# Kernel optimization log

Hardware: AMD Instinct MI355X
Metric: run time of the kernel (lower is better)

The kernel has to match this reference:

```python
import jax, jax.numpy as jnp
import numpy as np

B, T, D, H = 2, 2048, 1024, 16
DH = D // H


def setup_inputs() -> dict:
    key = jax.random.key(0)
    ks = jax.random.split(key, 8)
    s = 1.0 / np.sqrt(D)  # xavier-ish scale
    return {
        "query": jax.random.normal(ks[0], (B, T, D), jnp.float32),
        "key": jax.random.normal(ks[1], (B, T, D), jnp.float32),
        "value": jax.random.normal(ks[2], (B, T, D), jnp.float32),
        "Wq": jax.random.normal(ks[3], (D, D), jnp.float32) * s,
        "bq": jnp.zeros((D,), jnp.float32),
        "Wk": jax.random.normal(ks[4], (D, D), jnp.float32) * s,
        "bk": jnp.zeros((D,), jnp.float32),
        "Wv": jax.random.normal(ks[5], (D, D), jnp.float32) * s,
        "bv": jnp.zeros((D,), jnp.float32),
        "Wo": jax.random.normal(ks[6], (D, D), jnp.float32) * s,
        "bo": jnp.zeros((D,), jnp.float32),
        # causal mask (B, T, T); True = attend
        "mask": jnp.broadcast_to(jnp.tril(jnp.ones((T, T), bool)), (B, T, T)),
    }


def _split_heads(x):  # (B, T, D) -> (B, H, T, Dh)
    return x.reshape(B, T, H, DH).transpose(0, 2, 1, 3)


def reference(query, key, value, Wq, bq, Wk, bk, Wv, bv, Wo, bo, mask):
    q = _split_heads(query @ Wq + bq)
    k = _split_heads(key @ Wk + bk)
    v = _split_heads(value @ Wv + bv)
    scores = jnp.einsum("bhqd,bhkd->bhqk", q, k) / jnp.sqrt(jnp.float32(DH))
    scores = jnp.where(mask[:, None, :, :], scores, -jnp.inf)
    w = jax.nn.softmax(scores, axis=-1)
    out = jnp.einsum("bhqk,bhkd->bhqd", w, v)
    out = out.transpose(0, 2, 1, 3).reshape(B, T, D)  # merge heads
    return out @ Wo + bo
```

## Files before the change

kernel.cpp:

```cpp
#include <hip/hip_runtime.h>

typedef unsigned short u16;
typedef __attribute__((ext_vector_type(4))) float f32x4;
typedef __attribute__((ext_vector_type(8))) short bf16x8;

#define MFMA16(a,b,c) __builtin_amdgcn_mfma_f32_16x16x32_bf16((a),(b),(c),0,0,0)

__device__ inline u16 f2bf(float f){
  union { float f; unsigned u; } v; v.f = f;
  unsigned r = v.u + 0x7FFFu + ((v.u >> 16) & 1u);
  return (u16)(r >> 16);
}
__device__ inline u16 f2bf_fast(float f){
  union { float f; unsigned u; } v; v.f = f;
  return (u16)((v.u + 0x8000u) >> 16);
}

typedef const __attribute__((address_space(1))) unsigned int* gas_ptr;
typedef __attribute__((address_space(3))) unsigned int* las_ptr;
__device__ inline void gload_lds16(const u16* g, u16* l){
  __builtin_amdgcn_global_load_lds((gas_ptr)(const void*)g, (las_ptr)(void*)l, 16, 0, 0);
}

struct CvtArgs { const float* x[3]; u16* y[3]; };
__global__ void k_cvt3(CvtArgs a, int n4){
  const float* x = a.x[blockIdx.y];
  u16* y = a.y[blockIdx.y];
  int i = blockIdx.x*blockDim.x + threadIdx.x;
  if (i < n4){
    float4 v = ((const float4*)x)[i];
    ushort4 o;
    o.x = f2bf(v.x); o.y = f2bf(v.y); o.z = f2bf(v.z); o.w = f2bf(v.w);
    ((ushort4*)y)[i] = o;
  }
}

struct TwbArgs { const float* W[4]; u16* Wt[4]; };
__global__ void k_twb4(TwbArgs a){
  __shared__ u16 t[32][33];
  const float* W = a.W[blockIdx.z];
  u16* Wt = a.Wt[blockIdx.z];
  int kb = blockIdx.x*32, nb = blockIdx.y*32;
  int tx = threadIdx.x, ty = threadIdx.y;
  #pragma unroll
  for (int i=0;i<32;i+=8)
    t[ty+i][tx] = f2bf(W[(size_t)(kb+ty+i)*1024 + nb+tx]);
  __syncthreads();
  #pragma unroll
  for (int i=0;i<32;i+=8)
    Wt[(size_t)(nb+ty+i)*1024 + kb+tx] = t[tx][ty+i];
}

__global__ void k_tv(const u16* __restrict__ V, u16* __restrict__ VT){
  __shared__ u16 t[32][33];
  int tb = blockIdx.x*32;
  int db = blockIdx.y*32;
  int bh = blockIdx.z;
  int b = bh>>4, h = bh&15;
  int tx = threadIdx.x, ty = threadIdx.y;
  #pragma unroll
  for (int i=0;i<32;i+=8)
    t[ty+i][tx] = V[(size_t)(b*2048 + tb+ty+i)*1024 + h*64 + db+tx];
  __syncthreads();
  #pragma unroll
  for (int i=0;i<32;i+=8)
    VT[(size_t)(bh*64 + db+ty+i)*2048 + tb+tx] = t[tx][ty+i];
}

struct GemmArgs3 { const u16* A[3]; const u16* Bt[3]; const float* bias[3]; u16* C[3]; };
__global__ __launch_bounds__(256) void k_gemm3(GemmArgs3 g){
  const int N=1024, K=1024;
  int flat = blockIdx.x + (blockIdx.y<<5) + (blockIdx.z<<8);
  int swz = (flat&7)*96 + (flat>>3);
  int by = swz & 7, bx = (swz>>3) & 31, bz = swz >> 8;
  const u16* A = g.A[bz]; const u16* Bt = g.Bt[bz];
  const float* bias = g.bias[bz]; u16* C = g.C[bz];
  __shared__ __attribute__((aligned(16))) u16 As[128*64];
  __shared__ __attribute__((aligned(16))) u16 Bs[128*64];
  const int tid  = threadIdx.x;
  const int wave = tid>>6, lane = tid&63;
  const int lo = lane&15, hi = lane>>4;
  const int row0 = bx*128, col0 = by*128;
  const int wm = (wave>>1)*64, wn = (wave&1)*64;
  f32x4 acc[4][4];
  #pragma unroll
  for (int i=0;i<4;i++)
    #pragma unroll
    for (int j=0;j<4;j++) acc[i][j] = (f32x4){0.f,0.f,0.f,0.f};

  for (int k0=0; k0<K; k0+=64){
    #pragma unroll
    for (int r=0;r<4;r++){
      int c = r*256 + tid;
      gload_lds16(A  + (size_t)(row0 + (c>>3))*K + k0 + (c&7)*8, As + c*8);
      gload_lds16(Bt + (size_t)(col0 + (c>>3))*K + k0 + (c&7)*8, Bs + c*8);
    }
    __syncthreads();
    __builtin_amdgcn_s_setprio(1);
    #pragma unroll
    for (int ks=0;ks<2;ks++){
      bf16x8 af[4], bfr[4];
      #pragma unroll
      for (int mf=0;mf<4;mf++)
        af[mf] = *(const bf16x8*)(As + (wm+mf*16+lo)*64 + ks*32 + hi*8);
      #pragma unroll
      for (int nf=0;nf<4;nf++)
        bfr[nf] = *(const bf16x8*)(Bs + (wn+nf*16+lo)*64 + ks*32 + hi*8);
      #pragma unroll
      for (int mf=0;mf<4;mf++)
        #pragma unroll
        for (int nf=0;nf<4;nf++)
          acc[mf][nf] = MFMA16(af[mf], bfr[nf], acc[mf][nf]);
    }
    __builtin_amdgcn_s_setprio(0);
    __syncthreads();
  }
  #pragma unroll
  for (int mf=0;mf<4;mf++){
    #pragma unroll
    for (int nf=0;nf<4;nf++){
      int r0 = row0 + wm + mf*16 + hi*4;
      int c0 = col0 + wn + nf*16 + lo;
      float bv = bias[c0];
      #pragma unroll
      for (int r=0;r<4;r++)
        C[(size_t)(r0+r)*N + c0] = f2bf(acc[mf][nf][r] + bv);
    }
  }
}

__global__ __launch_bounds__(256) void k_gemmO(const u16* __restrict__ A, const u16* __restrict__ Bt,
                                               const float* __restrict__ bias, float* __restrict__ C){
  const int N=1024, K=1024;
  int f = blockIdx.x;
  int xcd = f & 7, idx = f >> 3;
  int bx = xcd*8 + (idx>>3), by = idx & 7;
  __shared__ __attribute__((aligned(16))) u16 As[64*64];
  __shared__ __attribute__((aligned(16))) u16 Bs[128*64];
  const int tid  = threadIdx.x;
  const int wave = tid>>6, lane = tid&63;
  const int lo = lane&15, hi = lane>>4;
  const int row0 = bx*64, col0 = by*128;
  const int wm = (wave>>1)*32, wn = (wave&1)*64;
  f32x4 acc[2][4];
  #pragma unroll
  for (int i=0;i<2;i++)
    #pragma unroll
    for (int j=0;j<4;j++) acc[i][j] = (f32x4){0.f,0.f,0.f,0.f};

  for (int k0=0; k0<K; k0+=64){
    #pragma unroll
    for (int r=0;r<2;r++){
      int c = r*256 + tid;
      gload_lds16(A + (size_t)(row0 + (c>>3))*K + k0 + (c&7)*8, As + c*8);
    }
    #pragma unroll
    for (int r=0;r<4;r++){
      int c = r*256 + tid;
      gload_lds16(Bt + (size_t)(col0 + (c>>3))*K + k0 + (c&7)*8, Bs + c*8);
    }
    __syncthreads();
    __builtin_amdgcn_s_setprio(1);
    #pragma unroll
    for (int ks=0;ks<2;ks++){
      bf16x8 af[2], bfr[4];
      #pragma unroll
      for (int mf=0;mf<2;mf++)
        af[mf] = *(const bf16x8*)(As + (wm+mf*16+lo)*64 + ks*32 + hi*8);
      #pragma unroll
      for (int nf=0;nf<4;nf++)
        bfr[nf] = *(const bf16x8*)(Bs + (wn+nf*16+lo)*64 + ks*32 + hi*8);
      #pragma unroll
      for (int mf=0;mf<2;mf++)
        #pragma unroll
        for (int nf=0;nf<4;nf++)
          acc[mf][nf] = MFMA16(af[mf], bfr[nf], acc[mf][nf]);
    }
    __builtin_amdgcn_s_setprio(0);
    __syncthreads();
  }
  #pragma unroll
  for (int mf=0;mf<2;mf++){
    #pragma unroll
    for (int nf=0;nf<4;nf++){
      int r0 = row0 + wm + mf*16 + hi*4;
      int c0 = col0 + wn + nf*16 + lo;
      float bv = bias[c0];
      #pragma unroll
      for (int r=0;r<4;r++)
        C[(size_t)(r0+r)*N + c0] = acc[mf][nf][r] + bv;
    }
  }
}

__global__ __launch_bounds__(256) void k_attn(
    const u16* __restrict__ Q, const u16* __restrict__ Kp,
    const u16* __restrict__ VT, u16* __restrict__ O)
{
  const int T=2048, D=1024;
  __shared__ __attribute__((aligned(16))) u16 Ks[2][64*64];
  __shared__ __attribute__((aligned(16))) u16 Vs[2][64*64];
  __shared__ __attribute__((aligned(16))) u16 Plds[4][16*64];
  int f = blockIdx.x + (blockIdx.y<<5);
  int xcd = f & 7, idx = f >> 3;
  const int bh = (xcd<<2) | (idx&3);
  const int qb = 31 - (idx>>2);
  const int b = bh>>4, h = bh&15;
  const int tid = threadIdx.x;
  const int wave = tid>>6, lane = tid&63;
  const int lo = lane&15, hi = lane>>4;
  const int wi = wave>>1, wj = wave&1;
  const int lo7 = lo&7;
  const float NEG = -1e30f;
  const float sc = 0.125f * 1.44269504f;
  const float MC = 64.0f * sc;
  const bf16x8 ones = {0x3F80,0x3F80,0x3F80,0x3F80,0x3F80,0x3F80,0x3F80,0x3F80};

  const int c0 = tid, c1 = 256 + tid;
  const int sr0 = c0>>3, sj0 = (c0&7)^(sr0&7);
  const int sr1 = c1>>3, sj1 = (c1&7)^(sr1&7);
  const u16* Kbase = Kp + (size_t)(b*T)*D + h*64;
  const u16* Vbase = VT + (size_t)(bh*64)*T;
  const size_t kOff0 = (size_t)sr0*D + sj0*8, kOff1 = (size_t)sr1*D + sj1*8;
  const size_t vOff0 = (size_t)sr0*T + sj0*8, vOff1 = (size_t)sr1*T + sj1*8;

  const int qrow0 = qb*64 + wi*32;
  bf16x8 qf[2][2];
  #pragma unroll
  for (int qnf=0;qnf<2;qnf++){
    const u16* Qr = Q + (size_t)(b*T + qrow0 + qnf*16 + lo)*D + h*64;
    qf[qnf][0] = *(const bf16x8*)(Qr + hi*8);
    qf[qnf][1] = *(const bf16x8*)(Qr + 32 + hi*8);
  }

  f32x4 o[2][4];
  #pragma unroll
  for (int i=0;i<2;i++)
    #pragma unroll
    for (int j=0;j<4;j++) o[i][j] = (f32x4){0.f,0.f,0.f,0.f};
  f32x4 lac[2];
  lac[0] = (f32x4){0.f,0.f,0.f,0.f};
  lac[1] = (f32x4){0.f,0.f,0.f,0.f};

  gload_lds16(Kbase + kOff0, &Ks[0][c0*8]);
  gload_lds16(Kbase + kOff1, &Ks[0][c1*8]);
  gload_lds16(Vbase + vOff0, &Vs[0][c0*8]);
  gload_lds16(Vbase + vOff1, &Vs[0][c1*8]);
  __syncthreads();

  u16* Pl = &Plds[wave][0];
  const int kcof0 = ((     hi) ^ lo7)*8;
  const int kcof1 = (( 4 + hi) ^ lo7)*8;
  const int vcof  = ((wj*4+hi) ^ lo7)*8;

  int cur = 0;
  for (int kb=0; kb<=qb; kb++){
    if (kb < qb){
      const u16* Kt = Kbase + (size_t)(kb+1)*64*D;
      const u16* Vt = Vbase + (kb+1)*64;
      gload_lds16(Kt + kOff0, &Ks[cur^1][c0*8]);
      gload_lds16(Kt + kOff1, &Ks[cur^1][c1*8]);
      gload_lds16(Vt + vOff0, &Vs[cur^1][c0*8]);
      gload_lds16(Vt + vOff1, &Vs[cur^1][c1*8]);
    }
    const u16* Kl = Ks[cur];
    const u16* Vl = Vs[cur];
    f32x4 s[2][2];
    __builtin_amdgcn_s_setprio(1);
    #pragma unroll
    for (int knf=0;knf<2;knf++){
      int krow = wj*32 + knf*16 + lo;
      bf16x8 kf0 = *(const bf16x8*)(Kl + krow*64 + kcof0);
      bf16x8 kf1 = *(const bf16x8*)(Kl + krow*64 + kcof1);
      #pragma unroll
      for (int qnf=0;qnf<2;qnf++){
        f32x4 z = (f32x4){0.f,0.f,0.f,0.f};
        z = MFMA16(kf0, qf[qnf][0], z);
        s[knf][qnf] = MFMA16(kf1, qf[qnf][1], z);
      }
    }
    __builtin_amdgcn_s_setprio(0);
    if (kb == qb){
      int ql = wi*32 + lo;
      #pragma unroll
      for (int knf=0;knf<2;knf++){
        int kl0 = wj*32 + knf*16 + 4*hi;
        #pragma unroll
        for (int qnf=0;qnf<2;qnf++){
          int qv = ql + qnf*16;
          #pragma unroll
          for (int r=0;r<4;r++)
            if (kl0 + r > qv) s[knf][qnf][r] = NEG;
        }
      }
    }
    #pragma unroll
    for (int knf=0;knf<2;knf++)
      #pragma unroll
      for (int qnf=0;qnf<2;qnf++){
        float p0 = __builtin_amdgcn_exp2f(__builtin_fmaf(s[knf][qnf][0], sc, -MC));
        float p1 = __builtin_amdgcn_exp2f(__builtin_fmaf(s[knf][qnf][1], sc, -MC));
        float p2 = __builtin_amdgcn_exp2f(__builtin_fmaf(s[knf][qnf][2], sc, -MC));
        float p3 = __builtin_amdgcn_exp2f(__builtin_fmaf(s[knf][qnf][3], sc, -MC));
        union { float f; unsigned u; } a0,a1,a2,a3;
        a0.f=p0; a1.f=p1; a2.f=p2; a3.f=p3;
        unsigned w0 = ((a0.u+0x8000u)>>16) | ((a1.u+0x8000u)&0xFFFF0000u);
        unsigned w1 = ((a2.u+0x8000u)>>16) | ((a3.u+0x8000u)&0xFFFF0000u);
        int gphys = (qnf*4 + knf*2 + (hi>>1)) ^ lo7;
        uint2 wv; wv.x = w0; wv.y = w1;
        *(uint2*)&Pl[lo*64 + gphys*8 + 4*(hi&1)] = wv;
      }
    bf16x8 pa0 = *(const bf16x8*)&Pl[lo*64 + kcof0];
    bf16x8 pa1 = *(const bf16x8*)&Pl[lo*64 + kcof1];
    __builtin_amdgcn_s_setprio(1);
    lac[0] = MFMA16(pa0, ones, lac[0]);
    lac[1] = MFMA16(pa1, ones, lac[1]);
    #pragma unroll
    for (int dhnf=0;dhnf<4;dhnf++){
      bf16x8 vf = *(const bf16x8*)(Vl + (dhnf*16+lo)*64 + vcof);
      o[0][dhnf] = MFMA16(pa0, vf, o[0][dhnf]);
      o[1][dhnf] = MFMA16(pa1, vf, o[1][dhnf]);
    }
    __builtin_amdgcn_s_setprio(0);
    __syncthreads();
    cur ^= 1;
  }
  float* os  = (float*)&Ks[0][0];
  float* lsc = (float*)&Vs[0][0];
  if (wj == 1){
    #pragma unroll
    for (int qnf=0;qnf<2;qnf++){
      #pragma unroll
      for (int dhnf=0;dhnf<4;dhnf++)
        #pragma unroll
        for (int r=0;r<4;r++)
          os[((wi*32 + qnf*16 + 4*hi + r)<<6) + dhnf*16 + lo] = o[qnf][dhnf][r];
      if (lo == 0)
        #pragma unroll
        for (int r=0;r<4;r++)
          lsc[wi*32 + qnf*16 + 4*hi + r] = lac[qnf][r];
    }
  }
  __syncthreads();
  if (wj == 0){
    #pragma unroll
    for (int qnf=0;qnf<2;qnf++)
      #pragma unroll
      for (int r=0;r<4;r++){
        int qloc = wi*32 + qnf*16 + 4*hi + r;
        float lt = lac[qnf][r] + lsc[qloc];
        float rinv = 1.0f / lt;
        #pragma unroll
        for (int dhnf=0;dhnf<4;dhnf++){
          float val = o[qnf][dhnf][r] + os[(qloc<<6) + dhnf*16 + lo];
          O[(size_t)(b*T + qb*64 + qloc)*D + h*64 + dhnf*16 + lo] = f2bf_fast(val * rinv);
        }
      }
  }
}

extern "C" void kernel_launch(void* const* d_in, const int* in_sizes, int n_in,
                              void* d_out, int out_size, void* d_ws, size_t ws_size,
                              hipStream_t stream) {
  const int B=2, T=2048, D=1024;
  const int M = B*T;
  const float* query = (const float*)d_in[0];
  const float* key   = (const float*)d_in[1];
  const float* value = (const float*)d_in[2];
  const float* Wq = (const float*)d_in[3];  const float* bq = (const float*)d_in[4];
  const float* Wk = (const float*)d_in[5];  const float* bk = (const float*)d_in[6];
  const float* Wv = (const float*)d_in[7];  const float* bv = (const float*)d_in[8];
  const float* Wo = (const float*)d_in[9];  const float* bo = (const float*)d_in[10];
  float* out = (float*)d_out;

  char* ws = (char*)d_ws;
  const size_t MB = 1024*1024;
  u16* xq  = (u16*)(ws + 0*MB);
  u16* xk  = (u16*)(ws + 8*MB);
  u16* xv  = (u16*)(ws + 16*MB);
  u16* WqT = (u16*)(ws + 24*MB);
  u16* WkT = (u16*)(ws + 26*MB);
  u16* WvT = (u16*)(ws + 28*MB);
  u16* WoT = (u16*)(ws + 30*MB);
  u16* Qp  = (u16*)(ws + 32*MB);
  u16* Kp  = (u16*)(ws + 40*MB);
  u16* Vp  = (u16*)(ws + 48*MB);
  u16* VTp = (u16*)(ws + 56*MB);
  u16* AO  = (u16*)(ws + 64*MB);

  int n4 = M*D/4;
  CvtArgs ca; ca.x[0]=query; ca.x[1]=key; ca.x[2]=value; ca.y[0]=xq; ca.y[1]=xk; ca.y[2]=xv;
  k_cvt3<<<dim3(n4/256, 3), 256, 0, stream>>>(ca, n4);

  TwbArgs ta; ta.W[0]=Wq; ta.W[1]=Wk; ta.W[2]=Wv; ta.W[3]=Wo;
  ta.Wt[0]=WqT; ta.Wt[1]=WkT; ta.Wt[2]=WvT; ta.Wt[3]=WoT;
  k_twb4<<<dim3(32,32,4), dim3(32,8), 0, stream>>>(ta);

  GemmArgs3 ga;
  ga.A[0]=xq; ga.A[1]=xk; ga.A[2]=xv;
  ga.Bt[0]=WqT; ga.Bt[1]=WkT; ga.Bt[2]=WvT;
  ga.bias[0]=bq; ga.bias[1]=bk; ga.bias[2]=bv;
  ga.C[0]=Qp; ga.C[1]=Kp; ga.C[2]=Vp;
  k_gemm3<<<dim3(32,8,3), 256, 0, stream>>>(ga);

  k_tv<<<dim3(T/32, 2, 32), dim3(32,8), 0, stream>>>(Vp, VTp);
  k_attn<<<dim3(32,32), 256, 0, stream>>>(Qp, Kp, VTp, AO);
  k_gemmO<<<512, 256, 0, stream>>>(AO, WoT, bo, out);
}
```

Baseline: 114.9 us.

## Fuse fp32-to-bf16 input conversion into QKV GEMM and swizzle LDS tiles

Measured after the change: 123.5 us. 1.07x slower.

```diff
diff --git a/kernel.cpp b/kernel.cpp
--- a/kernel.cpp
+++ b/kernel.cpp
@@ -15,24 +15,15 @@
   union { float f; unsigned u; } v; v.f = f;
   return (u16)((v.u + 0x8000u) >> 16);
 }
+__device__ inline unsigned pk2bf(float x, float y){
+  union { float f; unsigned u; } a, b; a.f=x; b.f=y;
+  return ((a.u + 0x8000u)>>16) | ((b.u + 0x8000u) & 0xFFFF0000u);
+}
 
 typedef const __attribute__((address_space(1))) unsigned int* gas_ptr;
 typedef __attribute__((address_space(3))) unsigned int* las_ptr;
 __device__ inline void gload_lds16(const u16* g, u16* l){
   __builtin_amdgcn_global_load_lds((gas_ptr)(const void*)g, (las_ptr)(void*)l, 16, 0, 0);
-}
-
-struct CvtArgs { const float* x[3]; u16* y[3]; };
-__global__ void k_cvt3(CvtArgs a, int n4){
-  const float* x = a.x[blockIdx.y];
-  u16* y = a.y[blockIdx.y];
-  int i = blockIdx.x*blockDim.x + threadIdx.x;
-  if (i < n4){
-    float4 v = ((const float4*)x)[i];
-    ushort4 o;
-    o.x = f2bf(v.x); o.y = f2bf(v.y); o.z = f2bf(v.z); o.w = f2bf(v.w);
-    ((ushort4*)y)[i] = o;
-  }
 }
 
 struct TwbArgs { const float* W[4]; u16* Wt[4]; };
@@ -67,19 +58,20 @@
     VT[(size_t)(bh*64 + db+ty+i)*2048 + tb+tx] = t[tx][ty+i];
 }
 
-struct GemmArgs3 { const u16* A[3]; const u16* Bt[3]; const float* bias[3]; u16* C[3]; };
+struct GemmArgs3 { const float* A[3]; const u16* Bt[3]; const float* bias[3]; u16* C[3]; };
 __global__ __launch_bounds__(256) void k_gemm3(GemmArgs3 g){
   const int N=1024, K=1024;
   int flat = blockIdx.x + (blockIdx.y<<5) + (blockIdx.z<<8);
   int swz = (flat&7)*96 + (flat>>3);
   int by = swz & 7, bx = (swz>>3) & 31, bz = swz >> 8;
-  const u16* A = g.A[bz]; const u16* Bt = g.Bt[bz];
+  const float* A = g.A[bz]; const u16* Bt = g.Bt[bz];
   const float* bias = g.bias[bz]; u16* C = g.C[bz];
-  __shared__ __attribute__((aligned(16))) u16 As[128*64];
-  __shared__ __attribute__((aligned(16))) u16 Bs[128*64];
+  __shared__ __attribute__((aligned(16))) float As[128*64];
+  __shared__ __attribute__((aligned(16))) u16   Bs[128*64];
   const int tid  = threadIdx.x;
   const int wave = tid>>6, lane = tid&63;
   const int lo = lane&15, hi = lane>>4;
+  const int lo7 = lo&7;
   const int row0 = bx*128, col0 = by*128;
   const int wm = (wave>>1)*64, wn = (wave&1)*64;
   f32x4 acc[4][4];
@@ -90,10 +82,16 @@
 
   for (int k0=0; k0<K; k0+=64){
     #pragma unroll
+    for (int r=0;r<8;r++){
+      int ga = r*256 + tid;
+      int sr = ga>>4, lg = (ga&15) ^ (sr&7);
+      gload_lds16((const u16*)(A + (size_t)(row0+sr)*K + k0 + lg*4), (u16*)(As + ga*4));
+    }
+    #pragma unroll
     for (int r=0;r<4;r++){
       int c = r*256 + tid;
-      gload_lds16(A  + (size_t)(row0 + (c>>3))*K + k0 + (c&7)*8, As + c*8);
-      gload_lds16(Bt + (size_t)(col0 + (c>>3))*K + k0 + (c&7)*8, Bs + c*8);
+      int sr = c>>3, lg = (c&7) ^ (sr&7);
+      gload_lds16(Bt + (size_t)(col0 + sr)*K + k0 + lg*8, Bs + c*8);
     }
     __syncthreads();
     __builtin_amdgcn_s_setprio(1);
@@ -101,11 +99,21 @@
     for (int ks=0;ks<2;ks++){
       bf16x8 af[4], bfr[4];
       #pragma unroll
-      for (int mf=0;mf<4;mf++)
-        af[mf] = *(const bf16x8*)(As + (wm+mf*16+lo)*64 + ks*32 + hi*8);
+      for (int mf=0;mf<4;mf++){
+        const float* Arow = As + (wm+mf*16+lo)*64;
+        int q0 = ks*8 + hi*2;
+        f32x4 a0 = *(const f32x4*)(Arow + ((q0  )^lo7)*4);
+        f32x4 a1 = *(const f32x4*)(Arow + ((q0+1)^lo7)*4);
+        union { unsigned u[4]; bf16x8 v; } pk;
+        pk.u[0] = pk2bf(a0[0], a0[1]);
+        pk.u[1] = pk2bf(a0[2], a0[3]);
+        pk.u[2] = pk2bf(a1[0], a1[1]);
+        pk.u[3] = pk2bf(a1[2], a1[3]);
+        af[mf] = pk.v;
+      }
       #pragma unroll
       for (int nf=0;nf<4;nf++)
-        bfr[nf] = *(const bf16x8*)(Bs + (wn+nf*16+lo)*64 + ks*32 + hi*8);
+        bfr[nf] = *(const bf16x8*)(Bs + (wn+nf*16+lo)*64 + ((ks*4+hi)^lo7)*8);
       #pragma unroll
       for (int mf=0;mf<4;mf++)
         #pragma unroll
@@ -302,10 +310,8 @@
         float p1 = __builtin_amdgcn_exp2f(__builtin_fmaf(s[knf][qnf][1], sc, -MC));
         float p2 = __builtin_amdgcn_exp2f(__builtin_fmaf(s[knf][qnf][2], sc, -MC));
         float p3 = __builtin_amdgcn_exp2f(__builtin_fmaf(s[knf][qnf][3], sc, -MC));
-        union { float f; unsigned u; } a0,a1,a2,a3;
-        a0.f=p0; a1.f=p1; a2.f=p2; a3.f=p3;
-        unsigned w0 = ((a0.u+0x8000u)>>16) | ((a1.u+0x8000u)&0xFFFF0000u);
-        unsigned w1 = ((a2.u+0x8000u)>>16) | ((a3.u+0x8000u)&0xFFFF0000u);
+        unsigned w0 = pk2bf(p0, p1);
+        unsigned w1 = pk2bf(p2, p3);
         int gphys = (qnf*4 + knf*2 + (hi>>1)) ^ lo7;
         uint2 wv; wv.x = w0; wv.y = w1;
         *(uint2*)&Pl[lo*64 + gphys*8 + 4*(hi&1)] = wv;
@@ -375,9 +381,6 @@
 
   char* ws = (char*)d_ws;
   const size_t MB = 1024*1024;
-  u16* xq  = (u16*)(ws + 0*MB);
-  u16* xk  = (u16*)(ws + 8*MB);
-  u16* xv  = (u16*)(ws + 16*MB);
   u16* WqT = (u16*)(ws + 24*MB);
   u16* WkT = (u16*)(ws + 26*MB);
   u16* WvT = (u16*)(ws + 28*MB);
@@ -388,16 +391,12 @@
   u16* VTp = (u16*)(ws + 56*MB);
   u16* AO  = (u16*)(ws + 64*MB);
 
-  int n4 = M*D/4;
-  CvtArgs ca; ca.x[0]=query; ca.x[1]=key; ca.x[2]=value; ca.y[0]=xq; ca.y[1]=xk; ca.y[2]=xv;
-  k_cvt3<<<dim3(n4/256, 3), 256, 0, stream>>>(ca, n4);
-
   TwbArgs ta; ta.W[0]=Wq; ta.W[1]=Wk; ta.W[2]=Wv; ta.W[3]=Wo;
   ta.Wt[0]=WqT; ta.Wt[1]=WkT; ta.Wt[2]=WvT; ta.Wt[3]=WoT;
   k_twb4<<<dim3(32,32,4), dim3(32,8), 0, stream>>>(ta);
 
   GemmArgs3 ga;
-  ga.A[0]=xq; ga.A[1]=xk; ga.A[2]=xv;
+  ga.A[0]=query; ga.A[1]=key; ga.A[2]=value;
   ga.Bt[0]=WqT; ga.Bt[1]=WkT; ga.Bt[2]=WvT;
   ga.bias[0]=bq; ga.bias[1]=bk; ga.bias[2]=bv;
   ga.C[0]=Qp; ga.C[1]=Kp; ga.C[2]=Vp;
```

## Rewrite QKV GEMM with 256x256 tiles and a 4-stage async LDS pipeline

Applied to the files above, without the earlier changes.

After: 116.5 us. Within noise of the previous version (+1.4%).

```diff
diff --git a/kernel.cpp b/kernel.cpp
--- a/kernel.cpp
+++ b/kernel.cpp
@@ -14,6 +14,10 @@
 __device__ inline u16 f2bf_fast(float f){
   union { float f; unsigned u; } v; v.f = f;
   return (u16)((v.u + 0x8000u) >> 16);
+}
+__device__ inline unsigned pk2bf(float x, float y){
+  union { float f; unsigned u; } a, b; a.f=x; b.f=y;
+  return ((a.u + 0x8000u)>>16) | ((b.u + 0x8000u) & 0xFFFF0000u);
 }
 
 typedef const __attribute__((address_space(1))) unsigned int* gas_ptr;
@@ -68,59 +72,108 @@
 }
 
 struct GemmArgs3 { const u16* A[3]; const u16* Bt[3]; const float* bias[3]; u16* C[3]; };
-__global__ __launch_bounds__(256) void k_gemm3(GemmArgs3 g){
-  const int N=1024, K=1024;
-  int flat = blockIdx.x + (blockIdx.y<<5) + (blockIdx.z<<8);
-  int swz = (flat&7)*96 + (flat>>3);
-  int by = swz & 7, bx = (swz>>3) & 31, bz = swz >> 8;
+
+#define STAGE_A(slot, kh) { \
+  int c0_ = tid, c1_ = tid + 512; \
+  gload_lds16(A + (size_t)(row0 + (c0_>>2))*1024 + (kh)*32 + (((c0_&3) ^ ((c0_>>3)&3))*8), &As[slot][c0_*8]); \
+  gload_lds16(A + (size_t)(row0 + (c1_>>2))*1024 + (kh)*32 + (((c1_&3) ^ ((c1_>>3)&3))*8), &As[slot][c1_*8]); }
+#define STAGE_B(slot, kh) { \
+  int c0_ = tid, c1_ = tid + 512; \
+  gload_lds16(Bt + (size_t)(col0 + (c0_>>2))*1024 + (kh)*32 + (((c0_&3) ^ ((c0_>>3)&3))*8), &Bs[slot][c0_*8]); \
+  gload_lds16(Bt + (size_t)(col0 + (c1_>>2))*1024 + (kh)*32 + (((c1_&3) ^ ((c1_>>3)&3))*8), &Bs[slot][c1_*8]); }
+
+#define KHALF_BODY(s) { \
+  const u16* Al = &As[s][0]; const u16* Bl = &Bs[s][0]; \
+  bf16x8 bfr[4], af[4]; \
+  _Pragma("unroll") \
+  for (int nf=0;nf<4;nf++) \
+    bfr[nf] = *(const bf16x8*)(Bl + (wc*64+nf*16+lo)*32 + pg*8); \
+  _Pragma("unroll") \
+  for (int mf=0;mf<4;mf++) \
+    af[mf] = *(const bf16x8*)(Al + (wr*128+mf*16+lo)*32 + pg*8); \
+  __builtin_amdgcn_s_setprio(1); \
+  _Pragma("unroll") \
+  for (int mf=0;mf<4;mf++) \
+    _Pragma("unroll") \
+    for (int nf=0;nf<4;nf++) \
+      acc[mf][nf] = MFMA16(af[mf], bfr[nf], acc[mf][nf]); \
+  __builtin_amdgcn_s_setprio(0); \
+  STAGE_B_GUARDED \
+  _Pragma("unroll") \
+  for (int mf=0;mf<4;mf++) \
+    af[mf] = *(const bf16x8*)(Al + (wr*128+(mf+4)*16+lo)*32 + pg*8); \
+  __builtin_amdgcn_s_setprio(1); \
+  _Pragma("unroll") \
+  for (int mf=0;mf<4;mf++) \
+    _Pragma("unroll") \
+    for (int nf=0;nf<4;nf++) \
+      acc[mf+4][nf] = MFMA16(af[mf], bfr[nf], acc[mf+4][nf]); \
+  __builtin_amdgcn_s_setprio(0); }
+
+__global__ __launch_bounds__(512) void k_gemm3(GemmArgs3 g){
+  const int N=1024;
+  __shared__ __attribute__((aligned(16))) u16 As[4][256*32];
+  __shared__ __attribute__((aligned(16))) u16 Bs[4][256*32];
+  int flat = blockIdx.x;
+  int swz = (flat&7)*24 + (flat>>3);
+  int bz = swz>>6, rem = swz&63;
+  int bx = rem>>2, by = rem&3;
   const u16* A = g.A[bz]; const u16* Bt = g.Bt[bz];
   const float* bias = g.bias[bz]; u16* C = g.C[bz];
-  __shared__ __attribute__((aligned(16))) u16 As[128*64];
-  __shared__ __attribute__((aligned(16))) u16 Bs[128*64];
-  const int tid  = threadIdx.x;
+  const int tid = threadIdx.x;
   const int wave = tid>>6, lane = tid&63;
   const int lo = lane&15, hi = lane>>4;
-  const int row0 = bx*128, col0 = by*128;
-  const int wm = (wave>>1)*64, wn = (wave&1)*64;
-  f32x4 acc[4][4];
-  #pragma unroll
-  for (int i=0;i<4;i++)
+  const int wr = wave>>2, wc = wave&3;
+  const int row0 = bx*256, col0 = by*256;
+  const int pg = hi ^ ((lo>>1)&3);
+
+  f32x4 acc[8][4];
+  #pragma unroll
+  for (int i=0;i<8;i++)
     #pragma unroll
     for (int j=0;j<4;j++) acc[i][j] = (f32x4){0.f,0.f,0.f,0.f};
 
-  for (int k0=0; k0<K; k0+=64){
-    #pragma unroll
-    for (int r=0;r<4;r++){
-      int c = r*256 + tid;
-      gload_lds16(A  + (size_t)(row0 + (c>>3))*K + k0 + (c&7)*8, As + c*8);
-      gload_lds16(Bt + (size_t)(col0 + (c>>3))*K + k0 + (c&7)*8, Bs + c*8);
-    }
-    __syncthreads();
-    __builtin_amdgcn_s_setprio(1);
-    #pragma unroll
-    for (int ks=0;ks<2;ks++){
-      bf16x8 af[4], bfr[4];
-      #pragma unroll
-      for (int mf=0;mf<4;mf++)
-        af[mf] = *(const bf16x8*)(As + (wm+mf*16+lo)*64 + ks*32 + hi*8);
-      #pragma unroll
-      for (int nf=0;nf<4;nf++)
-        bfr[nf] = *(const bf16x8*)(Bs + (wn+nf*16+lo)*64 + ks*32 + hi*8);
-      #pragma unroll
-      for (int mf=0;mf<4;mf++)
-        #pragma unroll
-        for (int nf=0;nf<4;nf++)
-          acc[mf][nf] = MFMA16(af[mf], bfr[nf], acc[mf][nf]);
-    }
-    __builtin_amdgcn_s_setprio(0);
-    __syncthreads();
-  }
-  #pragma unroll
-  for (int mf=0;mf<4;mf++){
+  STAGE_A(0,0); STAGE_B(0,0);
+  STAGE_A(1,1); STAGE_B(1,1);
+  STAGE_A(2,2); STAGE_B(2,2);
+
+  for (int h = 0; h < 29; ++h){
+    const int s = h & 3;
+    STAGE_A((h+3)&3, h+3);
+    asm volatile("s_waitcnt vmcnt(10)" ::: "memory");
+    __builtin_amdgcn_s_barrier();
+    #define STAGE_B_GUARDED STAGE_B((h+3)&3, h+3);
+    KHALF_BODY(s)
+    #undef STAGE_B_GUARDED
+  }
+  {
+    asm volatile("s_waitcnt vmcnt(8)" ::: "memory");
+    __builtin_amdgcn_s_barrier();
+    #define STAGE_B_GUARDED
+    KHALF_BODY(29&3)
+    #undef STAGE_B_GUARDED
+  }
+  {
+    asm volatile("s_waitcnt vmcnt(4)" ::: "memory");
+    __builtin_amdgcn_s_barrier();
+    #define STAGE_B_GUARDED
+    KHALF_BODY(30&3)
+    #undef STAGE_B_GUARDED
+  }
+  {
+    asm volatile("s_waitcnt vmcnt(0)" ::: "memory");
+    __builtin_amdgcn_s_barrier();
+    #define STAGE_B_GUARDED
+    KHALF_BODY(31&3)
+    #undef STAGE_B_GUARDED
+  }
+
+  #pragma unroll
+  for (int mf=0;mf<8;mf++){
     #pragma unroll
     for (int nf=0;nf<4;nf++){
-      int r0 = row0 + wm + mf*16 + hi*4;
-      int c0 = col0 + wn + nf*16 + lo;
+      int r0 = row0 + wr*128 + mf*16 + hi*4;
+      int c0 = col0 + wc*64 + nf*16 + lo;
       float bv = bias[c0];
       #pragma unroll
       for (int r=0;r<4;r++)
@@ -302,10 +355,8 @@
         float p1 = __builtin_amdgcn_exp2f(__builtin_fmaf(s[knf][qnf][1], sc, -MC));
         float p2 = __builtin_amdgcn_exp2f(__builtin_fmaf(s[knf][qnf][2], sc, -MC));
         float p3 = __builtin_amdgcn_exp2f(__builtin_fmaf(s[knf][qnf][3], sc, -MC));
-        union { float f; unsigned u; } a0,a1,a2,a3;
-        a0.f=p0; a1.f=p1; a2.f=p2; a3.f=p3;
-        unsigned w0 = ((a0.u+0x8000u)>>16) | ((a1.u+0x8000u)&0xFFFF0000u);
-        unsigned w1 = ((a2.u+0x8000u)>>16) | ((a3.u+0x8000u)&0xFFFF0000u);
+        unsigned w0 = pk2bf(p0, p1);
+        unsigned w1 = pk2bf(p2, p3);
         int gphys = (qnf*4 + knf*2 + (hi>>1)) ^ lo7;
         uint2 wv; wv.x = w0; wv.y = w1;
         *(uint2*)&Pl[lo*64 + gphys*8 + 4*(hi&1)] = wv;
@@ -401,7 +452,7 @@
   ga.Bt[0]=WqT; ga.Bt[1]=WkT; ga.Bt[2]=WvT;
   ga.bias[0]=bq; ga.bias[1]=bk; ga.bias[2]=bv;
   ga.C[0]=Qp; ga.C[1]=Kp; ga.C[2]=Vp;
-  k_gemm3<<<dim3(32,8,3), 256, 0, stream>>>(ga);
+  k_gemm3<<<192, 512, 0, stream>>>(ga);
 
   k_tv<<<dim3(T/32, 2, 32), dim3(32,8), 0, stream>>>(Vp, VTp);
   k_attn<<<dim3(32,32), 256, 0, stream>>>(Qp, Kp, VTp, AO);
```
